# Kernel optimization log

Measured on AMD Instinct MI355X. Metric: run time of the kernel, lower is better.

## Reference

```python
import jax, jax.numpy as jnp
import numpy as np

BATCH = 65536
IN_DIM = 512
LATENT = 32
NUM_TRIL = LATENT * (LATENT + 1) // 2  # 528
# torch.tril_indices returns row-major order, same as np.tril_indices
_ROWS, _COLS = np.tril_indices(LATENT)
ROWS = jnp.asarray(_ROWS)
COLS = jnp.asarray(_COLS)
BN_EPS = 1e-5
LRELU_SLOPE = 0.01


def setup_inputs() -> dict:
    key = jax.random.key(0)
    ks = jax.random.split(key, 12)
    x = jax.random.normal(ks[0], (BATCH, IN_DIM), dtype=jnp.float32)
    s_enc = 1.0 / np.sqrt(IN_DIM)
    s_lat = 1.0 / np.sqrt(LATENT)
    return {
        "x": x,
        "W_enc": jax.random.uniform(ks[1], (IN_DIM, LATENT), minval=-s_enc, maxval=s_enc, dtype=jnp.float32),
        "b_enc": jax.random.uniform(ks[2], (LATENT,), minval=-s_enc, maxval=s_enc, dtype=jnp.float32),
        "bn_gamma": jnp.ones((LATENT,), dtype=jnp.float32),
        "bn_beta": jnp.zeros((LATENT,), dtype=jnp.float32),
        "bn_mean": 0.1 * jax.random.normal(ks[3], (LATENT,), dtype=jnp.float32),
        "bn_var": jax.random.uniform(ks[4], (LATENT,), minval=0.5, maxval=1.5, dtype=jnp.float32),
        "W_mu": jax.random.uniform(ks[5], (LATENT, LATENT), minval=-s_lat, maxval=s_lat, dtype=jnp.float32),
        "b_mu": jax.random.uniform(ks[6], (LATENT,), minval=-s_lat, maxval=s_lat, dtype=jnp.float32),
        "W_ch": jax.random.uniform(ks[7], (LATENT, NUM_TRIL), minval=-s_lat, maxval=s_lat, dtype=jnp.float32),
        "b_ch": jax.random.uniform(ks[8], (NUM_TRIL,), minval=-s_lat, maxval=s_lat, dtype=jnp.float32),
    }


def _leaky_relu(v):
    return jnp.where(v >= 0, v, LRELU_SLOPE * v)


def reference(x, W_enc, b_enc, bn_gamma, bn_beta, bn_mean, bn_var, W_mu, b_mu, W_ch, b_ch):
    # downsampled_enc: Linear(512, latent) -> BatchNorm1d (eval mode) -> LeakyReLU
    h = x @ W_enc + b_enc                                        # [B, L]
    h = bn_gamma * (h - bn_mean) * jax.lax.rsqrt(bn_var + BN_EPS) + bn_beta
    h = _leaky_relu(h)
    # mu head
    mus = _leaky_relu(h @ W_mu + b_mu)                           # [B, L]
    # log-cholesky head -> 528 lower-triangular elements
    elts = _leaky_relu(h @ W_ch + b_ch)                          # [B, 528]
    B = x.shape[0]
    L = jnp.zeros((B, LATENT, LATENT), dtype=jnp.float32)
    L = L.at[:, ROWS, COLS].set(elts)                            # scatter into lower triangle
    di = jnp.arange(LATENT)
    diag = L[:, di, di]
    diag = jnp.clip(jax.nn.softplus(diag), 0.001, 100.0) + 0.01
    L = L.at[:, di, di].set(diag)
    # cov = L L^T + 0.01 I
    cov = jnp.einsum('bij,bkj->bik', L, L) + 0.01 * jnp.eye(LATENT, dtype=jnp.float32)
    return (h, mus, cov)
```

## Files before the change

kernel.cpp:

```cpp
#include <hip/hip_runtime.h>
#include <math.h>

constexpr int BATCH  = 65536;
constexpr int IN_DIM = 512;
constexpr int LATENT = 32;
constexpr int NTRIL  = 528;
constexpr float BN_EPS = 1e-5f;
constexpr float SLOPE  = 0.01f;

constexpr int RPB  = 64;
constexpr int SUBR = 8;
constexpr int HSTR = 36;
constexpr int LSTR = 36;
constexpr int LROW = LATENT * LSTR;
constexpr int PSTR = 36;

__device__ __forceinline__ float leaky(float v) {
    return v >= 0.0f ? v : SLOPE * v;
}

extern "C" __global__ __launch_bounds__(256, 4)
void enc_kernel(const float* __restrict__ x,
                const float* __restrict__ W_enc,
                const float* __restrict__ b_enc,
                const float* __restrict__ bn_gamma,
                const float* __restrict__ bn_beta,
                const float* __restrict__ bn_mean,
                const float* __restrict__ bn_var,
                float* __restrict__ h_out)
{
    __shared__ float part[4][RPB][PSTR];

    const int t = threadIdx.x;
    const int w = __builtin_amdgcn_readfirstlane(t >> 6);
    const int l = t & 63;
    const int row0 = blockIdx.x * RPB;

    {
        const float4* __restrict__ xp =
            (const float4*)(x + (size_t)(row0 + l) * IN_DIM + w * (IN_DIM / 4));
        const float* __restrict__ Wq = W_enc + (w * (IN_DIM / 4)) * LATENT;

        float acc[LATENT];
        #pragma unroll
        for (int c = 0; c < LATENT; ++c) acc[c] = 0.0f;

        float4 q0 = xp[0];
        float4 q1 = xp[1];
        #pragma unroll 2
        for (int k4 = 0; k4 < IN_DIM / 16; ++k4) {
            const float4 xv = q0;
            q0 = q1;
            const int pf = (k4 < IN_DIM / 16 - 2) ? (k4 + 2) : (IN_DIM / 16 - 1);
            q1 = xp[pf];

            const float* __restrict__ Wk = Wq + (4 * k4) * LATENT;
            #pragma unroll
            for (int c = 0; c < LATENT; ++c) acc[c] = fmaf(xv.x, Wk[c],            acc[c]);
            #pragma unroll
            for (int c = 0; c < LATENT; ++c) acc[c] = fmaf(xv.y, Wk[LATENT + c],   acc[c]);
            #pragma unroll
            for (int c = 0; c < LATENT; ++c) acc[c] = fmaf(xv.z, Wk[2*LATENT + c], acc[c]);
            #pragma unroll
            for (int c = 0; c < LATENT; ++c) acc[c] = fmaf(xv.w, Wk[3*LATENT + c], acc[c]);
        }

        #pragma unroll
        for (int c4 = 0; c4 < LATENT / 4; ++c4)
            *(float4*)&part[w][l][4 * c4] =
                make_float4(acc[4*c4+0], acc[4*c4+1], acc[4*c4+2], acc[4*c4+3]);
    }
    __syncthreads();

    {
        const int r  = t >> 2;
        const int c0 = (t & 3) * 8;
        float v[8];
        #pragma unroll
        for (int i = 0; i < 8; ++i) v[i] = 0.0f;
        #pragma unroll
        for (int ww = 0; ww < 4; ++ww) {
            const float4 p0 = *(const float4*)&part[ww][r][c0];
            const float4 p1 = *(const float4*)&part[ww][r][c0 + 4];
            v[0]+=p0.x; v[1]+=p0.y; v[2]+=p0.z; v[3]+=p0.w;
            v[4]+=p1.x; v[5]+=p1.y; v[6]+=p1.z; v[7]+=p1.w;
        }
        float hv[8];
        #pragma unroll
        for (int i = 0; i < 8; ++i) {
            const int c = c0 + i;
            float u = v[i] + b_enc[c];
            u = bn_gamma[c] * (u - bn_mean[c]) * rsqrtf(bn_var[c] + BN_EPS) + bn_beta[c];
            hv[i] = leaky(u);
        }
        float4* __restrict__ hp = (float4*)(h_out + (size_t)(row0 + r) * LATENT + c0);
        hp[0] = make_float4(hv[0], hv[1], hv[2], hv[3]);
        hp[1] = make_float4(hv[4], hv[5], hv[6], hv[7]);
    }
}

extern "C" __global__ __launch_bounds__(256)
void dec_kernel(const float* __restrict__ h_in,
                const float* __restrict__ W_mu,
                const float* __restrict__ b_mu,
                const float* __restrict__ W_ch,
                const float* __restrict__ b_ch,
                float* __restrict__ mu_out,
                float* __restrict__ cov_out)
{
    __shared__ float h_sh[RPB][HSTR];
    __shared__ float L_sh[SUBR][LROW];

    const int t = threadIdx.x;
    const int row0 = blockIdx.x * RPB;

    {
        const int r  = t >> 2;
        const int c0 = (t & 3) * 8;
        const float4* __restrict__ hg =
            (const float4*)(h_in + (size_t)(row0 + r) * LATENT + c0);
        const float4 a0 = hg[0];
        const float4 a1 = hg[1];
        *(float4*)&h_sh[r][c0]     = a0;
        *(float4*)&h_sh[r][c0 + 4] = a1;
    }
    __syncthreads();

    {
        const int c = t & 31;
        const int g = t >> 5;
        float wmu[LATENT];
        #pragma unroll
        for (int k = 0; k < LATENT; ++k) wmu[k] = W_mu[k * LATENT + c];
        const float bm = b_mu[c];
        #pragma unroll
        for (int j = 0; j < 8; ++j) {
            const int r = g * 8 + j;
            const float4* __restrict__ hr = (const float4*)&h_sh[r][0];
            float a = bm;
            #pragma unroll
            for (int k4 = 0; k4 < 8; ++k4) {
                const float4 hvv = hr[k4];
                a += hvv.x*wmu[4*k4+0] + hvv.y*wmu[4*k4+1]
                   + hvv.z*wmu[4*k4+2] + hvv.w*wmu[4*k4+3];
            }
            mu_out[(size_t)(row0 + r) * LATENT + c] = leaky(a);
        }
    }

    #pragma unroll 1
    for (int sb = 0; sb < RPB / SUBR; ++sb) {
        const int rbl = sb * SUBR;

        #pragma unroll 1
        for (int jid = t; jid < 2 * (NTRIL / 2); jid += 256) {
            const int q  = jid % (NTRIL / 2);
            const int rh = jid / (NTRIL / 2);
            const int j0 = 2 * q;

            float2 a[4];
            a[0] = make_float2(b_ch[j0], b_ch[j0 + 1]);
            a[1] = a[0]; a[2] = a[0]; a[3] = a[0];

            const float* __restrict__ wbase = W_ch + j0;
            #pragma unroll
            for (int kq = 0; kq < 8; ++kq) {
                float2 wv[4];
                #pragma unroll
                for (int e = 0; e < 4; ++e)
                    wv[e] = *(const float2*)(wbase + (4*kq + e) * NTRIL);
                #pragma unroll
                for (int rr = 0; rr < 4; ++rr) {
                    const float4 hvv = *(const float4*)&h_sh[rbl + rh*4 + rr][4*kq];
                    a[rr].x += hvv.x*wv[0].x + hvv.y*wv[1].x + hvv.z*wv[2].x + hvv.w*wv[3].x;
                    a[rr].y += hvv.x*wv[0].y + hvv.y*wv[1].y + hvv.z*wv[2].y + hvv.w*wv[3].y;
                }
            }

            #pragma unroll
            for (int e = 0; e < 2; ++e) {
                const int j = j0 + e;
                int ri = (int)((sqrtf(8.0f * (float)j + 1.0f) - 1.0f) * 0.5f);
                if ((ri + 1) * (ri + 2) / 2 <= j) ++ri;
                if (ri * (ri + 1) / 2 > j) --ri;
                const int ci = j - ri * (ri + 1) / 2;
                const bool isdiag = (ci == ri);
                #pragma unroll
                for (int rr = 0; rr < 4; ++rr) {
                    float vv = (e == 0) ? a[rr].x : a[rr].y;
                    vv = leaky(vv);
                    if (isdiag) {
                        float sp = vv > 20.0f ? vv : log1pf(__expf(vv));
                        vv = fminf(fmaxf(sp, 0.001f), 100.0f) + 0.01f;
                    }
                    L_sh[rh*4 + rr][ri * LSTR + ci] = vv;
                }
            }
        }
        __syncthreads();

        {
            const int lr = t >> 5;
            const int i  = t & 31;
            const float* __restrict__ Lrow = &L_sh[lr][0];

            float Li[LATENT];
            #pragma unroll
            for (int j = 0; j < LATENT; ++j) {
                const float v = Lrow[i * LSTR + j];
                Li[j] = (j <= i) ? v : 0.0f;
            }

            float cr[LATENT];
            #pragma unroll
            for (int k = 0; k < LATENT; ++k) {
                float a = 0.0f;
                const float* __restrict__ Lk = Lrow + k * LSTR;
                #pragma unroll
                for (int qq = 0; 4 * qq <= k; ++qq) {
                    const float4 wv = *(const float4*)(Lk + 4 * qq);
                    if (4*qq + 0 <= k) a += Li[4*qq+0] * wv.x;
                    if (4*qq + 1 <= k) a += Li[4*qq+1] * wv.y;
                    if (4*qq + 2 <= k) a += Li[4*qq+2] * wv.z;
                    if (4*qq + 3 <= k) a += Li[4*qq+3] * wv.w;
                }
                cr[k] = (k == i) ? a + 0.01f : a;
            }

            const size_t grow = (size_t)(row0 + rbl + lr);
            float4* __restrict__ cp =
                (float4*)(cov_out + grow * (size_t)(LATENT * LATENT) + (size_t)i * LATENT);
            #pragma unroll
            for (int k4 = 0; k4 < 8; ++k4)
                cp[k4] = make_float4(cr[4*k4+0], cr[4*k4+1], cr[4*k4+2], cr[4*k4+3]);
        }
        __syncthreads();
    }
}

extern "C" void kernel_launch(void* const* d_in, const int* in_sizes, int n_in,
                              void* d_out, int out_size, void* d_ws, size_t ws_size,
                              hipStream_t stream) {
    const float* x        = (const float*)d_in[0];
    const float* W_enc    = (const float*)d_in[1];
    const float* b_enc    = (const float*)d_in[2];
    const float* bn_gamma = (const float*)d_in[3];
    const float* bn_beta  = (const float*)d_in[4];
    const float* bn_mean  = (const float*)d_in[5];
    const float* bn_var   = (const float*)d_in[6];
    const float* W_mu     = (const float*)d_in[7];
    const float* b_mu     = (const float*)d_in[8];
    const float* W_ch     = (const float*)d_in[9];
    const float* b_ch     = (const float*)d_in[10];
    float* out = (float*)d_out;

    float* h_out   = out;
    float* mu_out  = out + (size_t)BATCH * LATENT;
    float* cov_out = out + (size_t)2 * BATCH * LATENT;

    enc_kernel<<<dim3(BATCH / RPB), dim3(256), 0, stream>>>(
        x, W_enc, b_enc, bn_gamma, bn_beta, bn_mean, bn_var, h_out);
    dec_kernel<<<dim3(BATCH / RPB), dim3(256), 0, stream>>>(
        h_out, W_mu, b_mu, W_ch, b_ch, mu_out, cov_out);
}
```

Baseline: 689.4 us.

## Pack L in padded triangular shared layout and balance Cholesky-product work per thread

Stores the lower-triangular factor in a packed, 4-aligned, zero-padded shared-memory layout, which lets 16 rows be processed per sub-block instead of 8. Each thread in the L·L^T stage now handles one short and one long row (p and p+16) to balance the triangular work. Cov rows are written as float4 as they are produced, so no full 32-element register array is held. The head GEMM is also re-tiled to 4 outputs × 2 rows per thread with float4 weight loads. The cost is more registers per thread and a one-time zeroing pass over shared memory.

```diff
diff --git a/kernel.cpp b/kernel.cpp
--- a/kernel.cpp
+++ b/kernel.cpp
@@ -9,11 +9,16 @@
 constexpr float SLOPE  = 0.01f;
 
 constexpr int RPB  = 64;
-constexpr int SUBR = 8;
+constexpr int SUBR = 16;
 constexpr int HSTR = 36;
-constexpr int LSTR = 36;
-constexpr int LROW = LATENT * LSTR;
 constexpr int PSTR = 36;
+
+constexpr int LSTRIDE = 584;
+
+__device__ __host__ __forceinline__ constexpr int rstart(int i) {
+    const int g = i >> 2, r = i & 3;
+    return 4 * (i + 2 * g * (g - 1) + r * g);
+}
 
 __device__ __forceinline__ float leaky(float v) {
     return v >= 0.0f ? v : SLOPE * v;
@@ -109,10 +114,17 @@
                 float* __restrict__ cov_out)
 {
     __shared__ float h_sh[RPB][HSTR];
-    __shared__ float L_sh[SUBR][LROW];
+    __shared__ float L_sh[SUBR * LSTRIDE];
 
     const int t = threadIdx.x;
     const int row0 = blockIdx.x * RPB;
+
+    {
+        float4* z4 = (float4*)L_sh;
+        const float4 z = make_float4(0.f, 0.f, 0.f, 0.f);
+        #pragma unroll 1
+        for (int s = t; s < SUBR * LSTRIDE / 4; s += 256) z4[s] = z;
+    }
 
     {
         const int r  = t >> 2;
@@ -153,86 +165,121 @@
         const int rbl = sb * SUBR;
 
         #pragma unroll 1
-        for (int jid = t; jid < 2 * (NTRIL / 2); jid += 256) {
-            const int q  = jid % (NTRIL / 2);
-            const int rh = jid / (NTRIL / 2);
-            const int j0 = 2 * q;
-
-            float2 a[4];
-            a[0] = make_float2(b_ch[j0], b_ch[j0 + 1]);
-            a[1] = a[0]; a[2] = a[0]; a[3] = a[0];
+        for (int jid = t; jid < 132 * 8; jid += 256) {
+            const int q  = jid % 132;
+            const int rg = jid / 132;
+            const int j0 = 4 * q;
+            const int r0s = rbl + rg * 2;
+
+            float4 a0 = make_float4(b_ch[j0+0], b_ch[j0+1], b_ch[j0+2], b_ch[j0+3]);
+            float4 a1 = a0;
 
             const float* __restrict__ wbase = W_ch + j0;
             #pragma unroll
             for (int kq = 0; kq < 8; ++kq) {
-                float2 wv[4];
-                #pragma unroll
-                for (int e = 0; e < 4; ++e)
-                    wv[e] = *(const float2*)(wbase + (4*kq + e) * NTRIL);
-                #pragma unroll
-                for (int rr = 0; rr < 4; ++rr) {
-                    const float4 hvv = *(const float4*)&h_sh[rbl + rh*4 + rr][4*kq];
-                    a[rr].x += hvv.x*wv[0].x + hvv.y*wv[1].x + hvv.z*wv[2].x + hvv.w*wv[3].x;
-                    a[rr].y += hvv.x*wv[0].y + hvv.y*wv[1].y + hvv.z*wv[2].y + hvv.w*wv[3].y;
-                }
-            }
-
-            #pragma unroll
-            for (int e = 0; e < 2; ++e) {
+                const float4 w0 = *(const float4*)(wbase + (4*kq + 0) * NTRIL);
+                const float4 w1 = *(const float4*)(wbase + (4*kq + 1) * NTRIL);
+                const float4 w2 = *(const float4*)(wbase + (4*kq + 2) * NTRIL);
+                const float4 w3 = *(const float4*)(wbase + (4*kq + 3) * NTRIL);
+                const float4 h0 = *(const float4*)&h_sh[r0s    ][4*kq];
+                const float4 h1 = *(const float4*)&h_sh[r0s + 1][4*kq];
+                a0.x += h0.x*w0.x + h0.y*w1.x + h0.z*w2.x + h0.w*w3.x;
+                a0.y += h0.x*w0.y + h0.y*w1.y + h0.z*w2.y + h0.w*w3.y;
+                a0.z += h0.x*w0.z + h0.y*w1.z + h0.z*w2.z + h0.w*w3.z;
+                a0.w += h0.x*w0.w + h0.y*w1.w + h0.z*w2.w + h0.w*w3.w;
+                a1.x += h1.x*w0.x + h1.y*w1.x + h1.z*w2.x + h1.w*w3.x;
+                a1.y += h1.x*w0.y + h1.y*w1.y + h1.z*w2.y + h1.w*w3.y;
+                a1.z += h1.x*w0.z + h1.y*w1.z + h1.z*w2.z + h1.w*w3.z;
+                a1.w += h1.x*w0.w + h1.y*w1.w + h1.z*w2.w + h1.w*w3.w;
+            }
+
+            #pragma unroll
+            for (int e = 0; e < 4; ++e) {
                 const int j = j0 + e;
                 int ri = (int)((sqrtf(8.0f * (float)j + 1.0f) - 1.0f) * 0.5f);
                 if ((ri + 1) * (ri + 2) / 2 <= j) ++ri;
                 if (ri * (ri + 1) / 2 > j) --ri;
                 const int ci = j - ri * (ri + 1) / 2;
                 const bool isdiag = (ci == ri);
+                const int off = rstart(ri) + ci;
+
+                float v0 = (e == 0) ? a0.x : (e == 1) ? a0.y : (e == 2) ? a0.z : a0.w;
+                float v1 = (e == 0) ? a1.x : (e == 1) ? a1.y : (e == 2) ? a1.z : a1.w;
+                v0 = leaky(v0);
+                v1 = leaky(v1);
+                if (isdiag) {
+                    float s0 = v0 > 20.0f ? v0 : log1pf(__expf(v0));
+                    float s1 = v1 > 20.0f ? v1 : log1pf(__expf(v1));
+                    v0 = fminf(fmaxf(s0, 0.001f), 100.0f) + 0.01f;
+                    v1 = fminf(fmaxf(s1, 0.001f), 100.0f) + 0.01f;
+                }
+                L_sh[(r0s - rbl) * LSTRIDE + off]       = v0;
+                L_sh[(r0s - rbl + 1) * LSTRIDE + off]   = v1;
+            }
+        }
+        __syncthreads();
+
+        {
+            const int lr = t >> 4;
+            const int p  = t & 15;
+            const float* __restrict__ Lb = L_sh + lr * LSTRIDE;
+
+            float a0[16];
+            {
+                const int s0 = rstart(p);
                 #pragma unroll
-                for (int rr = 0; rr < 4; ++rr) {
-                    float vv = (e == 0) ? a[rr].x : a[rr].y;
-                    vv = leaky(vv);
-                    if (isdiag) {
-                        float sp = vv > 20.0f ? vv : log1pf(__expf(vv));
-                        vv = fminf(fmaxf(sp, 0.001f), 100.0f) + 0.01f;
+                for (int qq = 0; qq < 4; ++qq) {
+                    const float4 v = *(const float4*)(Lb + s0 + 4*qq);
+                    a0[4*qq+0] = (4*qq+0 <= p) ? v.x : 0.0f;
+                    a0[4*qq+1] = (4*qq+1 <= p) ? v.y : 0.0f;
+                    a0[4*qq+2] = (4*qq+2 <= p) ? v.z : 0.0f;
+                    a0[4*qq+3] = (4*qq+3 <= p) ? v.w : 0.0f;
+                }
+            }
+            float a1[32];
+            {
+                const int i1 = p + 16;
+                const int s1 = rstart(i1);
+                #pragma unroll
+                for (int qq = 0; qq < 8; ++qq) {
+                    const float4 v = *(const float4*)(Lb + s1 + 4*qq);
+                    a1[4*qq+0] = (4*qq+0 <= i1) ? v.x : 0.0f;
+                    a1[4*qq+1] = (4*qq+1 <= i1) ? v.y : 0.0f;
+                    a1[4*qq+2] = (4*qq+2 <= i1) ? v.z : 0.0f;
+                    a1[4*qq+3] = (4*qq+3 <= i1) ? v.w : 0.0f;
+                }
+            }
+
+            const size_t grow = (size_t)(row0 + rbl + lr);
+            float* __restrict__ cov0 =
+                cov_out + grow * (size_t)(LATENT * LATENT) + (size_t)p * LATENT;
+            float* __restrict__ cov1 = cov0 + 16 * LATENT;
+
+            float c0[4], c1[4];
+            #pragma unroll
+            for (int k = 0; k < LATENT; ++k) {
+                const int qk = (k >> 2) + 1;
+                const float* __restrict__ Lk = Lb + rstart(k);
+                float d0 = 0.0f, d1 = 0.0f;
+                #pragma unroll
+                for (int qq = 0; qq < qk; ++qq) {
+                    const float4 w = *(const float4*)(Lk + 4*qq);
+                    if (qq < 4) {
+                        d0 += a0[4*qq+0]*w.x + a0[4*qq+1]*w.y
+                            + a0[4*qq+2]*w.z + a0[4*qq+3]*w.w;
                     }
-                    L_sh[rh*4 + rr][ri * LSTR + ci] = vv;
-                }
-            }
-        }
-        __syncthreads();
-
-        {
-            const int lr = t >> 5;
-            const int i  = t & 31;
-            const float* __restrict__ Lrow = &L_sh[lr][0];
-
-            float Li[LATENT];
-            #pragma unroll
-            for (int j = 0; j < LATENT; ++j) {
-                const float v = Lrow[i * LSTR + j];
-                Li[j] = (j <= i) ? v : 0.0f;
-            }
-
-            float cr[LATENT];
-            #pragma unroll
-            for (int k = 0; k < LATENT; ++k) {
-                float a = 0.0f;
-                const float* __restrict__ Lk = Lrow + k * LSTR;
-                #pragma unroll
-                for (int qq = 0; 4 * qq <= k; ++qq) {
-                    const float4 wv = *(const float4*)(Lk + 4 * qq);
-                    if (4*qq + 0 <= k) a += Li[4*qq+0] * wv.x;
-                    if (4*qq + 1 <= k) a += Li[4*qq+1] * wv.y;
-                    if (4*qq + 2 <= k) a += Li[4*qq+2] * wv.z;
-                    if (4*qq + 3 <= k) a += Li[4*qq+3] * wv.w;
-                }
-                cr[k] = (k == i) ? a + 0.01f : a;
-            }
-
-            const size_t grow = (size_t)(row0 + rbl + lr);
-            float4* __restrict__ cp =
-                (float4*)(cov_out + grow * (size_t)(LATENT * LATENT) + (size_t)i * LATENT);
-            #pragma unroll
-            for (int k4 = 0; k4 < 8; ++k4)
-                cp[k4] = make_float4(cr[4*k4+0], cr[4*k4+1], cr[4*k4+2], cr[4*k4+3]);
+                    d1 += a1[4*qq+0]*w.x + a1[4*qq+1]*w.y
+                        + a1[4*qq+2]*w.z + a1[4*qq+3]*w.w;
+                }
+                d0 = (k == p)      ? d0 + 0.01f : d0;
+                d1 = (k == p + 16) ? d1 + 0.01f : d1;
+                c0[k & 3] = d0;
+                c1[k & 3] = d1;
+                if ((k & 3) == 3) {
+                    *(float4*)(cov0 + (k - 3)) = make_float4(c0[0], c0[1], c0[2], c0[3]);
+                    *(float4*)(cov1 + (k - 3)) = make_float4(c1[0], c1[1], c1[2], c1[3]);
+                }
+            }
         }
         __syncthreads();
     }
```

New measurement: 672.0 us. -2.5%, faster.
